# Performance work log

Hardware: AMD Instinct MI355X
Metric: run time of the kernel (lower is better)

Reference implementation:

```python
import jax, jax.numpy as jnp
import numpy as np

N_USER = 100000
N_ITEM = 100000
N_EDGE = 1600000
HID = 64
IN_U = 128
IN_I = 64
N_LAYERS = 2


def setup_inputs() -> dict:
    key = jax.random.key(0)
    ks = jax.random.split(key, 12)
    s = 0.05
    return {
        "x_user": jax.random.normal(ks[0], (N_USER, IN_U), jnp.float32),
        "x_item": jax.random.normal(ks[1], (N_ITEM, IN_I), jnp.float32),
        "edge_ui": jax.random.randint(ks[2], (2, N_EDGE), 0, N_USER),  # row0 src(user), row1 dst(item)
        "edge_iu": jax.random.randint(ks[3], (2, N_EDGE), 0, N_ITEM),  # row0 src(item), row1 dst(user)
        "Wu": jax.random.normal(ks[4], (IN_U, HID), jnp.float32) * s,
        "bu": jnp.zeros((HID,), jnp.float32),
        "Wi": jax.random.normal(ks[5], (IN_I, HID), jnp.float32) * s,
        "bi": jnp.zeros((HID,), jnp.float32),
        "Wl": jax.random.normal(ks[6], (N_LAYERS, 2, HID, HID), jnp.float32) * s,
        "bl": jnp.zeros((N_LAYERS, 2, HID), jnp.float32),
        "Wr": jax.random.normal(ks[7], (N_LAYERS, 2, HID, HID), jnp.float32) * s,
    }


def _sage(h_src, h_dst, edge, Wl, bl, Wr, n_dst):
    # SAGEConv: mean-aggregate gathered source features, then lin_l(agg)+bias + lin_r(dst)
    src, dst = edge[0], edge[1]
    msg = h_src[src]  # [E, HID] gather
    agg = jax.ops.segment_sum(msg, dst, num_segments=n_dst)
    cnt = jax.ops.segment_sum(jnp.ones((edge.shape[1], 1), h_src.dtype), dst, num_segments=n_dst)
    mean = agg / jnp.maximum(cnt, 1.0)
    return mean @ Wl + bl + h_dst @ Wr


def reference(x_user, x_item, edge_ui, edge_iu, Wu, bu, Wi, bi, Wl, bl, Wr):
    # per-node-type input linear + relu (dropout = identity at inference)
    hu = jax.nn.relu(x_user @ Wu + bu)
    hi = jax.nn.relu(x_item @ Wi + bi)
    for l in range(N_LAYERS):
        # edge type 0: user -> item ; edge type 1: item -> user ; HeteroConv aggr='sum'
        new_i = _sage(hu, hi, edge_ui, Wl[l, 0], bl[l, 0], Wr[l, 0], N_ITEM)
        new_u = _sage(hi, hu, edge_iu, Wl[l, 1], bl[l, 1], Wr[l, 1], N_USER)
        hu = jax.nn.relu(new_u)
        hi = jax.nn.relu(new_i)
    return hu, hi
```

## Files before the change

kernel.cpp:

```cpp
#include <hip/hip_runtime.h>

#define NUSER 100000
#define NITEM 100000
#define NEDGE 1600000
#define HID 64
#define NPB 256
#define NBKT 391
#define ACHUNK 8192
#define NCHUNK ((NEDGE + ACHUNK - 1) / ACHUNK)

__device__ __forceinline__ unsigned short f2bf(float x) {
  unsigned int u; __builtin_memcpy(&u, &x, 4);
  u += 0x7fffu + ((u >> 16) & 1u);
  return (unsigned short)(u >> 16);
}
__device__ __forceinline__ float bflo(unsigned int u) {
  unsigned int v = u << 16; float f; __builtin_memcpy(&f, &v, 4); return f;
}
__device__ __forceinline__ float bfhi(unsigned int u) {
  unsigned int v = u & 0xffff0000u; float f; __builtin_memcpy(&f, &v, 4); return f;
}

template<int K>
__global__ __launch_bounds__(256) void gemm64(
    const float* __restrict__ A, const float* __restrict__ W,
    const float* __restrict__ bias, float* __restrict__ C, int M)
{
  __shared__ float Ws[K * 64];
  __shared__ float As[64 * 68];
  const int tid = threadIdx.x;

  for (int i = tid; i < K * 16; i += 256)
    ((float4*)Ws)[i] = ((const float4*)W)[i];

  const int tx = tid & 15;
  const int ty = tid >> 4;
  float4 bv = ((const float4*)bias)[tx];

  const int ntiles = (M + 63) >> 6;
  for (int t = blockIdx.x; t < ntiles; t += gridDim.x) {
    const int row0 = t << 6;
    float acc[4][4] = {};
    for (int kb = 0; kb < K; kb += 64) {
      __syncthreads();
      for (int i = tid; i < 1024; i += 256) {
        int r = i >> 4;
        int kk = (i & 15) << 2;
        int gr = row0 + r; if (gr > M - 1) gr = M - 1;
        *(float4*)&As[r * 68 + kk] = *(const float4*)(A + (size_t)gr * K + kb + kk);
      }
      __syncthreads();
      #pragma unroll 8
      for (int k = 0; k < 64; ++k) {
        float4 w = *(const float4*)&Ws[(kb + k) * 64 + tx * 4];
        float a0 = As[(ty * 4 + 0) * 68 + k];
        float a1 = As[(ty * 4 + 1) * 68 + k];
        float a2 = As[(ty * 4 + 2) * 68 + k];
        float a3 = As[(ty * 4 + 3) * 68 + k];
        acc[0][0] += a0 * w.x; acc[0][1] += a0 * w.y; acc[0][2] += a0 * w.z; acc[0][3] += a0 * w.w;
        acc[1][0] += a1 * w.x; acc[1][1] += a1 * w.y; acc[1][2] += a1 * w.z; acc[1][3] += a1 * w.w;
        acc[2][0] += a2 * w.x; acc[2][1] += a2 * w.y; acc[2][2] += a2 * w.z; acc[2][3] += a2 * w.w;
        acc[3][0] += a3 * w.x; acc[3][1] += a3 * w.y; acc[3][2] += a3 * w.z; acc[3][3] += a3 * w.w;
      }
    }
    #pragma unroll
    for (int r = 0; r < 4; ++r) {
      int gr = row0 + ty * 4 + r;
      if (gr < M) {
        float4 o = make_float4(fmaxf(acc[r][0] + bv.x, 0.f), fmaxf(acc[r][1] + bv.y, 0.f),
                               fmaxf(acc[r][2] + bv.z, 0.f), fmaxf(acc[r][3] + bv.w, 0.f));
        *(float4*)(C + (size_t)gr * 64 + tx * 4) = o;
      }
    }
  }
}

__global__ __launch_bounds__(256) void gemm_dual2(
    const float* A0, const float* __restrict__ Wa0, const float* __restrict__ Wb0,
    const float* __restrict__ bias0, unsigned short* Ga0, float* Tb0,
    const float* A1, const float* __restrict__ Wa1, const float* __restrict__ Wb1,
    const float* __restrict__ bias1, unsigned short* Ga1, float* Tb1,
    int M, int half_blocks)
{
  __shared__ float Ws[64 * 128];
  __shared__ float As[64 * 68];
  const int tid = threadIdx.x;

  const float* A; const float* Wa; const float* Wb; const float* bias;
  unsigned short* Ga; float* Tb; int t;
  if ((int)blockIdx.x < half_blocks) {
    A = A0; Wa = Wa0; Wb = Wb0; bias = bias0; Ga = Ga0; Tb = Tb0; t = blockIdx.x;
  } else {
    A = A1; Wa = Wa1; Wb = Wb1; bias = bias1; Ga = Ga1; Tb = Tb1; t = blockIdx.x - half_blocks;
  }

  for (int i = tid; i < 2048; i += 256) {
    int k = i >> 5, cg = i & 31;
    float4 v = (cg < 16) ? ((const float4*)Wa)[k * 16 + cg]
                         : ((const float4*)Wb)[k * 16 + (cg - 16)];
    ((float4*)Ws)[k * 32 + cg] = v;
  }

  const int tx = tid & 15;
  const int ty = tid >> 4;
  float4 bvB = ((const float4*)bias)[tx];

  const int row0 = t << 6;
  float accA[4][4] = {};
  float accB[4][4] = {};
  __syncthreads();
  for (int i = tid; i < 1024; i += 256) {
    int r = i >> 4;
    int kk = (i & 15) << 2;
    int gr = row0 + r; if (gr > M - 1) gr = M - 1;
    *(float4*)&As[r * 68 + kk] = *(const float4*)(A + (size_t)gr * 64 + kk);
  }
  __syncthreads();
  #pragma unroll 8
  for (int k = 0; k < 64; ++k) {
    float4 wa = *(const float4*)&Ws[k * 128 + tx * 4];
    float4 wb = *(const float4*)&Ws[k * 128 + 64 + tx * 4];
    float a0 = As[(ty * 4 + 0) * 68 + k];
    float a1 = As[(ty * 4 + 1) * 68 + k];
    float a2 = As[(ty * 4 + 2) * 68 + k];
    float a3 = As[(ty * 4 + 3) * 68 + k];
    accA[0][0] += a0 * wa.x; accA[0][1] += a0 * wa.y; accA[0][2] += a0 * wa.z; accA[0][3] += a0 * wa.w;
    accA[1][0] += a1 * wa.x; accA[1][1] += a1 * wa.y; accA[1][2] += a1 * wa.z; accA[1][3] += a1 * wa.w;
    accA[2][0] += a2 * wa.x; accA[2][1] += a2 * wa.y; accA[2][2] += a2 * wa.z; accA[2][3] += a2 * wa.w;
    accA[3][0] += a3 * wa.x; accA[3][1] += a3 * wa.y; accA[3][2] += a3 * wa.z; accA[3][3] += a3 * wa.w;
    accB[0][0] += a0 * wb.x; accB[0][1] += a0 * wb.y; accB[0][2] += a0 * wb.z; accB[0][3] += a0 * wb.w;
    accB[1][0] += a1 * wb.x; accB[1][1] += a1 * wb.y; accB[1][2] += a1 * wb.z; accB[1][3] += a1 * wb.w;
    accB[2][0] += a2 * wb.x; accB[2][1] += a2 * wb.y; accB[2][2] += a2 * wb.z; accB[2][3] += a2 * wb.w;
    accB[3][0] += a3 * wb.x; accB[3][1] += a3 * wb.y; accB[3][2] += a3 * wb.z; accB[3][3] += a3 * wb.w;
  }
  #pragma unroll
  for (int r = 0; r < 4; ++r) {
    int gr = row0 + ty * 4 + r;
    if (gr < M) {
      ushort4 g;
      g.x = f2bf(accA[r][0]); g.y = f2bf(accA[r][1]);
      g.z = f2bf(accA[r][2]); g.w = f2bf(accA[r][3]);
      *(ushort4*)(Ga + (size_t)gr * 64 + tx * 4) = g;
      *(float4*)(Tb + (size_t)gr * 64 + tx * 4) =
          make_float4(accB[r][0] + bvB.x, accB[r][1] + bvB.y,
                      accB[r][2] + bvB.z, accB[r][3] + bvB.w);
    }
  }
}

__global__ __launch_bounds__(256) void agg2(
    const unsigned short* __restrict__ G0, const float* T0,
    const int* __restrict__ ptr0, const int* __restrict__ idx0, float* out0,
    const unsigned short* __restrict__ G1, const float* T1,
    const int* __restrict__ ptr1, const int* __restrict__ idx1, float* out1,
    int n_dst)
{
  const int lane = threadIdx.x & 63;
  const int sub = lane >> 5;
  const int ch = (lane & 31) << 1;
  int wave = blockIdx.x * 4 + (threadIdx.x >> 6);
  const int nwh = (gridDim.x * 4) >> 1;
  const unsigned short* G; const float* T; const int* ptr; const int* idx; float* out;
  if (wave < nwh) { G = G0; T = T0; ptr = ptr0; idx = idx0; out = out0; }
  else { G = G1; T = T1; ptr = ptr1; idx = idx1; out = out1; wave -= nwh; }

  for (int n0 = wave * 2; n0 < n_dst; n0 += nwh * 2) {
    const int n = n0 + sub;
    const bool valid = n < n_dst;
    const int s = valid ? ptr[n] : 0;
    const int e = valid ? ptr[n + 1] : 0;
    float2 t = make_float2(0.f, 0.f);
    if (valid) t = *(const float2*)(T + (size_t)n * 64 + ch);
    float l0 = 0.f, h0 = 0.f, l1 = 0.f, h1 = 0.f;
    float l2 = 0.f, h2 = 0.f, l3 = 0.f, h3 = 0.f;
    float l4 = 0.f, h4 = 0.f, l5 = 0.f, h5 = 0.f;
    float l6 = 0.f, h6 = 0.f, l7 = 0.f, h7 = 0.f;
    int i = s;
    for (; i + 8 <= e; i += 8) {
      int j0 = __builtin_nontemporal_load(idx + i + 0);
      int j1 = __builtin_nontemporal_load(idx + i + 1);
      int j2 = __builtin_nontemporal_load(idx + i + 2);
      int j3 = __builtin_nontemporal_load(idx + i + 3);
      int j4 = __builtin_nontemporal_load(idx + i + 4);
      int j5 = __builtin_nontemporal_load(idx + i + 5);
      int j6 = __builtin_nontemporal_load(idx + i + 6);
      int j7 = __builtin_nontemporal_load(idx + i + 7);
      unsigned int g0 = *(const unsigned int*)(G + (size_t)j0 * 64 + ch);
      unsigned int g1 = *(const unsigned int*)(G + (size_t)j1 * 64 + ch);
      unsigned int g2 = *(const unsigned int*)(G + (size_t)j2 * 64 + ch);
      unsigned int g3 = *(const unsigned int*)(G + (size_t)j3 * 64 + ch);
      unsigned int g4 = *(const unsigned int*)(G + (size_t)j4 * 64 + ch);
      unsigned int g5 = *(const unsigned int*)(G + (size_t)j5 * 64 + ch);
      unsigned int g6 = *(const unsigned int*)(G + (size_t)j6 * 64 + ch);
      unsigned int g7 = *(const unsigned int*)(G + (size_t)j7 * 64 + ch);
      l0 += bflo(g0); h0 += bfhi(g0); l1 += bflo(g1); h1 += bfhi(g1);
      l2 += bflo(g2); h2 += bfhi(g2); l3 += bflo(g3); h3 += bfhi(g3);
      l4 += bflo(g4); h4 += bfhi(g4); l5 += bflo(g5); h5 += bfhi(g5);
      l6 += bflo(g6); h6 += bfhi(g6); l7 += bflo(g7); h7 += bfhi(g7);
    }
    for (; i < e; ++i) {
      int j = __builtin_nontemporal_load(idx + i);
      unsigned int g = *(const unsigned int*)(G + (size_t)j * 64 + ch);
      l0 += bflo(g); h0 += bfhi(g);
    }
    float sl = ((l0 + l1) + (l2 + l3)) + ((l4 + l5) + (l6 + l7));
    float sh = ((h0 + h1) + (h2 + h3)) + ((h4 + h5) + (h6 + h7));
    int deg = e - s;
    float inv = 1.f / (float)(deg > 0 ? deg : 1);
    if (valid) {
      float2 o = make_float2(fmaxf(sl * inv + t.x, 0.f), fmaxf(sh * inv + t.y, 0.f));
      *(float2*)(out + (size_t)n * 64 + ch) = o;
    }
  }
}

__global__ __launch_bounds__(256) void bucket_hist(
    const int* __restrict__ dstA, const int* __restrict__ dstB,
    int* histA, int* histB, int E)
{
  __shared__ int h[NBKT];
  for (int i = threadIdx.x; i < NBKT; i += 256) h[i] = 0;
  __syncthreads();
  const int half = gridDim.x >> 1;
  const bool isB = (int)blockIdx.x >= half;
  const int* dst = isB ? dstB : dstA;
  int* hist = isB ? histB : histA;
  const int b0 = isB ? blockIdx.x - half : blockIdx.x;
  for (int e = b0 * 256 + (int)threadIdx.x; e < E; e += half * 256)
    atomicAdd(&h[__builtin_nontemporal_load(dst + e) >> 8], 1);
  __syncthreads();
  for (int i = threadIdx.x; i < NBKT; i += 256)
    if (h[i]) atomicAdd(&hist[i], h[i]);
}

__global__ __launch_bounds__(512) void bucket_scan(
    const int* __restrict__ histA, const int* __restrict__ histB,
    int* baseA, int* curA, int* baseB, int* curB,
    int* ptrA_end, int* ptrB_end, int E)
{
  __shared__ int sA[512], sB[512];
  const int t = threadIdx.x;
  int vA = (t < NBKT) ? histA[t] : 0;
  int vB = (t < NBKT) ? histB[t] : 0;
  sA[t] = vA; sB[t] = vB;
  __syncthreads();
  for (int off = 1; off < 512; off <<= 1) {
    int xA = 0, xB = 0;
    if (t >= off) { xA = sA[t - off]; xB = sB[t - off]; }
    __syncthreads();
    if (t >= off) { sA[t] += xA; sB[t] += xB; }
    __syncthreads();
  }
  if (t < NBKT) {
    int eA = sA[t] - vA, eB = sB[t] - vB;
    baseA[t] = eA; curA[t] = eA;
    baseB[t] = eB; curB[t] = eB;
  }
  if (t == 0) {
    baseA[NBKT] = E; baseB[NBKT] = E;
    *ptrA_end = E; *ptrB_end = E;
  }
}

__global__ __launch_bounds__(256) void partition2(
    const int* __restrict__ srcA, const int* __restrict__ dstA, int* curA, unsigned int* pairsA,
    const int* __restrict__ srcB, const int* __restrict__ dstB, int* curB, unsigned int* pairsB,
    int E)
{
  __shared__ int h[NBKT];
  __shared__ int c[NBKT];
  const int half = gridDim.x >> 1;
  const bool isB = (int)blockIdx.x >= half;
  const int chunk = isB ? blockIdx.x - half : blockIdx.x;
  const int* src = isB ? srcB : srcA;
  const int* dst = isB ? dstB : dstA;
  int* cur = isB ? curB : curA;
  unsigned int* pairs = isB ? pairsB : pairsA;
  const int e0 = chunk * ACHUNK;
  const int e1 = min(e0 + ACHUNK, E);
  for (int i = threadIdx.x; i < NBKT; i += 256) h[i] = 0;
  __syncthreads();
  for (int e = e0 + (int)threadIdx.x; e < e1; e += 256)
    atomicAdd(&h[__builtin_nontemporal_load(dst + e) >> 8], 1);
  __syncthreads();
  for (int i = threadIdx.x; i < NBKT; i += 256) {
    int v = h[i];
    if (v) c[i] = atomicAdd(&cur[i], v);
  }
  __syncthreads();
  for (int e = e0 + (int)threadIdx.x; e < e1; e += 256) {
    int d = __builtin_nontemporal_load(dst + e);
    int s = __builtin_nontemporal_load(src + e);
    int b = d >> 8;
    int p = atomicAdd(&c[b], 1);
    pairs[p] = ((unsigned int)(d & 255) << 24) | (unsigned int)s;
  }
}

__global__ __launch_bounds__(256) void bucket_fill(
    const unsigned int* __restrict__ pairsA, const int* __restrict__ baseA,
    int* __restrict__ ptrA, int* __restrict__ idxA,
    const unsigned int* __restrict__ pairsB, const int* __restrict__ baseB,
    int* __restrict__ ptrB, int* __restrict__ idxB, int n)
{
  __shared__ int h[NPB];
  __shared__ int cur[NPB];
  const bool isB = (int)blockIdx.x >= NBKT;
  const int b = isB ? blockIdx.x - NBKT : blockIdx.x;
  const unsigned int* pairs = isB ? pairsB : pairsA;
  const int* base = isB ? baseB : baseA;
  int* ptr = isB ? ptrB : ptrA;
  int* idx = isB ? idxB : idxA;
  const int ebase = base[b];
  const int eend = base[b + 1];
  const int t = threadIdx.x;
  h[t] = 0;
  __syncthreads();
  for (int e = ebase + t; e < eend; e += 256)
    atomicAdd(&h[pairs[e] >> 24], 1);
  __syncthreads();
  const int v = h[t];
  __syncthreads();
  for (int off = 1; off < 256; off <<= 1) {
    int x = 0;
    if (t >= off) x = h[t - off];
    __syncthreads();
    if (t >= off) h[t] += x;
    __syncthreads();
  }
  const int excl = h[t] - v;
  const int gnode = b * NPB + t;
  if (gnode < n) ptr[gnode] = ebase + excl;
  cur[t] = excl;
  __syncthreads();
  for (int e = ebase + t; e < eend; e += 256) {
    unsigned int pk = pairs[e];
    int p = atomicAdd(&cur[pk >> 24], 1);
    idx[ebase + p] = (int)(pk & 0xFFFFFFu);
  }
}

extern "C" void kernel_launch(void* const* d_in, const int* in_sizes, int n_in,
                              void* d_out, int out_size, void* d_ws, size_t ws_size,
                              hipStream_t stream) {
  const float* x_user = (const float*)d_in[0];
  const float* x_item = (const float*)d_in[1];
  const int*   edge_ui = (const int*)d_in[2];
  const int*   edge_iu = (const int*)d_in[3];
  const float* Wu = (const float*)d_in[4];
  const float* bu = (const float*)d_in[5];
  const float* Wi = (const float*)d_in[6];
  const float* bi = (const float*)d_in[7];
  const float* Wl = (const float*)d_in[8];
  const float* bl = (const float*)d_in[9];
  const float* Wr = (const float*)d_in[10];

  float* outU = (float*)d_out;
  float* outI = outU + (size_t)NUSER * HID;

  char* p = (char*)d_ws;
  auto alloc = [&](size_t bytes) -> void* {
    void* r = (void*)p; p += (bytes + 255) & ~(size_t)255; return r;
  };
  float* U = (float*)alloc((size_t)NUSER * HID * 4);
  float* I = (float*)alloc((size_t)NITEM * HID * 4);
  unsigned short* GA = (unsigned short*)alloc((size_t)NUSER * HID * 2);
  unsigned short* GB = (unsigned short*)alloc((size_t)NITEM * HID * 2);
  unsigned int* pairsA = (unsigned int*)GA;
  unsigned int* pairsB = pairsA + NEDGE;
  int* histA = (int*)alloc((size_t)(2 * NBKT + 2 * (NBKT + 1) + 2 * NBKT) * 4);
  int* histB = histA + NBKT;
  int* baseA = histB + NBKT;
  int* baseB = baseA + NBKT + 1;
  int* curA  = baseB + NBKT + 1;
  int* curB  = curA + NBKT;
  int* ptr_ui = (int*)alloc(((size_t)NITEM + 1) * 4);
  int* ptr_iu = (int*)alloc(((size_t)NUSER + 1) * 4);
  int* idx_ui = (int*)alloc((size_t)NEDGE * 4);
  int* idx_iu = (int*)alloc((size_t)NEDGE * 4);

  hipMemsetAsync(histA, 0, (size_t)(2 * NBKT) * 4, stream);
  bucket_hist<<<784, 256, 0, stream>>>(edge_ui + NEDGE, edge_iu + NEDGE,
                                       histA, histB, NEDGE);
  bucket_scan<<<1, 512, 0, stream>>>(histA, histB, baseA, curA, baseB, curB,
                                     ptr_ui + NITEM, ptr_iu + NUSER, NEDGE);
  partition2<<<2 * NCHUNK, 256, 0, stream>>>(
      edge_ui, edge_ui + NEDGE, curA, pairsA,
      edge_iu, edge_iu + NEDGE, curB, pairsB, NEDGE);
  bucket_fill<<<2 * NBKT, 256, 0, stream>>>(pairsA, baseA, ptr_ui, idx_ui,
                                            pairsB, baseB, ptr_iu, idx_iu, NITEM);

  const int GT = (NUSER + 63) / 64;
  const int AGG_B = 2 * ((NUSER / 2 + 3) / 4);

  const float* Wl00 = Wl;             const float* Wl01 = Wl + 4096;
  const float* Wl10 = Wl + 2 * 4096;  const float* Wl11 = Wl + 3 * 4096;
  const float* Wr00 = Wr;             const float* Wr01 = Wr + 4096;
  const float* Wr10 = Wr + 2 * 4096;  const float* Wr11 = Wr + 3 * 4096;
  const float* bl00 = bl;             const float* bl01 = bl + 64;
  const float* bl10 = bl + 128;       const float* bl11 = bl + 192;

  gemm64<128><<<GT, 256, 0, stream>>>(x_user, Wu, bu, U, NUSER);
  gemm64<64 ><<<GT, 256, 0, stream>>>(x_item, Wi, bi, I, NITEM);

  gemm_dual2<<<2 * GT, 256, 0, stream>>>(U, Wl00, Wr01, bl01, GA, outU,
                                         I, Wl01, Wr00, bl00, GB, outI,
                                         NUSER, GT);
  agg2<<<AGG_B, 256, 0, stream>>>(GA, outI, ptr_ui, idx_ui, outI,
                                  GB, outU, ptr_iu, idx_iu, outU, NITEM);

  gemm_dual2<<<2 * GT, 256, 0, stream>>>(outI, Wl11, Wr10, bl10, GA, outI,
                                         outU, Wl10, Wr11, bl11, GB, outU,
                                         NITEM, GT);
  agg2<<<AGG_B, 256, 0, stream>>>(GA, outU, ptr_iu, idx_iu, outU,
                                  GB, outI, ptr_ui, idx_ui, outI, NUSER);
}
```

Baseline: 609.2 us.

## Schedule aggregation by XCD affinity with atomic work-stealing chunks

Replaces the static split of waves between the two edge directions with dynamic chunk claiming through per-side global atomic counters. Each block reads its XCD id and processes the side assigned to its XCD half first, so each half of the chip keeps one gathered feature table hot in its L2 before switching to the other side. This adds an atomic plus two block barriers per 64-node chunk and relies on the hardware XCC_ID register.

```diff
diff --git a/kernel.cpp b/kernel.cpp
--- a/kernel.cpp
+++ b/kernel.cpp
@@ -8,6 +8,7 @@
 #define NBKT 391
 #define ACHUNK 8192
 #define NCHUNK ((NEDGE + ACHUNK - 1) / ACHUNK)
+#define AGGCH 64
 
 __device__ __forceinline__ unsigned short f2bf(float x) {
   unsigned int u; __builtin_memcpy(&u, &x, 4);
@@ -19,6 +20,11 @@
 }
 __device__ __forceinline__ float bfhi(unsigned int u) {
   unsigned int v = u & 0xffff0000u; float f; __builtin_memcpy(&f, &v, 4); return f;
+}
+__device__ __forceinline__ int xcd_id() {
+  int x;
+  asm volatile("s_getreg_b32 %0, hwreg(HW_REG_XCC_ID)" : "=s"(x));
+  return x & 7;
 }
 
 template<int K>
@@ -153,63 +159,80 @@
     const int* __restrict__ ptr0, const int* __restrict__ idx0, float* out0,
     const unsigned short* __restrict__ G1, const float* T1,
     const int* __restrict__ ptr1, const int* __restrict__ idx1, float* out1,
-    int n_dst)
+    int* wc, int n_dst)
 {
   const int lane = threadIdx.x & 63;
   const int sub = lane >> 5;
   const int ch = (lane & 31) << 1;
-  int wave = blockIdx.x * 4 + (threadIdx.x >> 6);
-  const int nwh = (gridDim.x * 4) >> 1;
-  const unsigned short* G; const float* T; const int* ptr; const int* idx; float* out;
-  if (wave < nwh) { G = G0; T = T0; ptr = ptr0; idx = idx0; out = out0; }
-  else { G = G1; T = T1; ptr = ptr1; idx = idx1; out = out1; wave -= nwh; }
-
-  for (int n0 = wave * 2; n0 < n_dst; n0 += nwh * 2) {
-    const int n = n0 + sub;
-    const bool valid = n < n_dst;
-    const int s = valid ? ptr[n] : 0;
-    const int e = valid ? ptr[n + 1] : 0;
-    float2 t = make_float2(0.f, 0.f);
-    if (valid) t = *(const float2*)(T + (size_t)n * 64 + ch);
-    float l0 = 0.f, h0 = 0.f, l1 = 0.f, h1 = 0.f;
-    float l2 = 0.f, h2 = 0.f, l3 = 0.f, h3 = 0.f;
-    float l4 = 0.f, h4 = 0.f, l5 = 0.f, h5 = 0.f;
-    float l6 = 0.f, h6 = 0.f, l7 = 0.f, h7 = 0.f;
-    int i = s;
-    for (; i + 8 <= e; i += 8) {
-      int j0 = __builtin_nontemporal_load(idx + i + 0);
-      int j1 = __builtin_nontemporal_load(idx + i + 1);
-      int j2 = __builtin_nontemporal_load(idx + i + 2);
-      int j3 = __builtin_nontemporal_load(idx + i + 3);
-      int j4 = __builtin_nontemporal_load(idx + i + 4);
-      int j5 = __builtin_nontemporal_load(idx + i + 5);
-      int j6 = __builtin_nontemporal_load(idx + i + 6);
-      int j7 = __builtin_nontemporal_load(idx + i + 7);
-      unsigned int g0 = *(const unsigned int*)(G + (size_t)j0 * 64 + ch);
-      unsigned int g1 = *(const unsigned int*)(G + (size_t)j1 * 64 + ch);
-      unsigned int g2 = *(const unsigned int*)(G + (size_t)j2 * 64 + ch);
-      unsigned int g3 = *(const unsigned int*)(G + (size_t)j3 * 64 + ch);
-      unsigned int g4 = *(const unsigned int*)(G + (size_t)j4 * 64 + ch);
-      unsigned int g5 = *(const unsigned int*)(G + (size_t)j5 * 64 + ch);
-      unsigned int g6 = *(const unsigned int*)(G + (size_t)j6 * 64 + ch);
-      unsigned int g7 = *(const unsigned int*)(G + (size_t)j7 * 64 + ch);
-      l0 += bflo(g0); h0 += bfhi(g0); l1 += bflo(g1); h1 += bfhi(g1);
-      l2 += bflo(g2); h2 += bfhi(g2); l3 += bflo(g3); h3 += bfhi(g3);
-      l4 += bflo(g4); h4 += bfhi(g4); l5 += bflo(g5); h5 += bfhi(g5);
-      l6 += bflo(g6); h6 += bfhi(g6); l7 += bflo(g7); h7 += bfhi(g7);
-    }
-    for (; i < e; ++i) {
-      int j = __builtin_nontemporal_load(idx + i);
-      unsigned int g = *(const unsigned int*)(G + (size_t)j * 64 + ch);
-      l0 += bflo(g); h0 += bfhi(g);
-    }
-    float sl = ((l0 + l1) + (l2 + l3)) + ((l4 + l5) + (l6 + l7));
-    float sh = ((h0 + h1) + (h2 + h3)) + ((h4 + h5) + (h6 + h7));
-    int deg = e - s;
-    float inv = 1.f / (float)(deg > 0 ? deg : 1);
-    if (valid) {
-      float2 o = make_float2(fmaxf(sl * inv + t.x, 0.f), fmaxf(sh * inv + t.y, 0.f));
-      *(float2*)(out + (size_t)n * 64 + ch) = o;
+  const int slot = ((threadIdx.x >> 6) << 1) | sub;
+  const int nchk = (n_dst + AGGCH - 1) / AGGCH;
+  const int g = xcd_id();
+  __shared__ int s_c;
+
+  for (int pass = 0; pass < 2; ++pass) {
+    const int side = ((g >> 2) ^ pass) & 1;
+    const unsigned short* G = side ? G1 : G0;
+    const float* T = side ? T1 : T0;
+    const int* ptr = side ? ptr1 : ptr0;
+    const int* idx = side ? idx1 : idx0;
+    float* out = side ? out1 : out0;
+    int* cnt = wc + side;
+    for (;;) {
+      if (threadIdx.x == 0) s_c = atomicAdd(cnt, 1);
+      __syncthreads();
+      const int c = s_c;
+      __syncthreads();
+      if (c >= nchk) break;
+      const int base = c * AGGCH;
+      #pragma unroll 1
+      for (int it = 0; it < AGGCH / 8; ++it) {
+        const int n = base + it * 8 + slot;
+        const bool valid = n < n_dst;
+        const int s = valid ? ptr[n] : 0;
+        const int e = valid ? ptr[n + 1] : 0;
+        float2 t = make_float2(0.f, 0.f);
+        if (valid) t = *(const float2*)(T + (size_t)n * 64 + ch);
+        float l0 = 0.f, h0 = 0.f, l1 = 0.f, h1 = 0.f;
+        float l2 = 0.f, h2 = 0.f, l3 = 0.f, h3 = 0.f;
+        float l4 = 0.f, h4 = 0.f, l5 = 0.f, h5 = 0.f;
+        float l6 = 0.f, h6 = 0.f, l7 = 0.f, h7 = 0.f;
+        int i = s;
+        for (; i + 8 <= e; i += 8) {
+          int j0 = __builtin_nontemporal_load(idx + i + 0);
+          int j1 = __builtin_nontemporal_load(idx + i + 1);
+          int j2 = __builtin_nontemporal_load(idx + i + 2);
+          int j3 = __builtin_nontemporal_load(idx + i + 3);
+          int j4 = __builtin_nontemporal_load(idx + i + 4);
+          int j5 = __builtin_nontemporal_load(idx + i + 5);
+          int j6 = __builtin_nontemporal_load(idx + i + 6);
+          int j7 = __builtin_nontemporal_load(idx + i + 7);
+          unsigned int g0 = *(const unsigned int*)(G + (size_t)j0 * 64 + ch);
+          unsigned int g1 = *(const unsigned int*)(G + (size_t)j1 * 64 + ch);
+          unsigned int g2 = *(const unsigned int*)(G + (size_t)j2 * 64 + ch);
+          unsigned int g3 = *(const unsigned int*)(G + (size_t)j3 * 64 + ch);
+          unsigned int g4 = *(const unsigned int*)(G + (size_t)j4 * 64 + ch);
+          unsigned int g5 = *(const unsigned int*)(G + (size_t)j5 * 64 + ch);
+          unsigned int g6 = *(const unsigned int*)(G + (size_t)j6 * 64 + ch);
+          unsigned int g7 = *(const unsigned int*)(G + (size_t)j7 * 64 + ch);
+          l0 += bflo(g0); h0 += bfhi(g0); l1 += bflo(g1); h1 += bfhi(g1);
+          l2 += bflo(g2); h2 += bfhi(g2); l3 += bflo(g3); h3 += bfhi(g3);
+          l4 += bflo(g4); h4 += bfhi(g4); l5 += bflo(g5); h5 += bfhi(g5);
+          l6 += bflo(g6); h6 += bfhi(g6); l7 += bflo(g7); h7 += bfhi(g7);
+        }
+        for (; i < e; ++i) {
+          int j = __builtin_nontemporal_load(idx + i);
+          unsigned int gv = *(const unsigned int*)(G + (size_t)j * 64 + ch);
+          l0 += bflo(gv); h0 += bfhi(gv);
+        }
+        float sl = ((l0 + l1) + (l2 + l3)) + ((l4 + l5) + (l6 + l7));
+        float sh = ((h0 + h1) + (h2 + h3)) + ((h4 + h5) + (h6 + h7));
+        int deg = e - s;
+        float inv = 1.f / (float)(deg > 0 ? deg : 1);
+        if (valid) {
+          float2 o = make_float2(fmaxf(sl * inv + t.x, 0.f), fmaxf(sh * inv + t.y, 0.f));
+          *(float2*)(out + (size_t)n * 64 + ch) = o;
+        }
+      }
     }
   }
 }
@@ -368,9 +391,10 @@
   unsigned short* GB = (unsigned short*)alloc((size_t)NITEM * HID * 2);
   unsigned int* pairsA = (unsigned int*)GA;
   unsigned int* pairsB = pairsA + NEDGE;
-  int* histA = (int*)alloc((size_t)(2 * NBKT + 2 * (NBKT + 1) + 2 * NBKT) * 4);
+  int* histA = (int*)alloc((size_t)(2 * NBKT + 8 + 2 * (NBKT + 1) + 2 * NBKT) * 4);
   int* histB = histA + NBKT;
-  int* baseA = histB + NBKT;
+  int* wc    = histA + 2 * NBKT;
+  int* baseA = wc + 8;
   int* baseB = baseA + NBKT + 1;
   int* curA  = baseB + NBKT + 1;
   int* curB  = curA + NBKT;
@@ -379,7 +403,7 @@
   int* idx_ui = (int*)alloc((size_t)NEDGE * 4);
   int* idx_iu = (int*)alloc((size_t)NEDGE * 4);
 
-  hipMemsetAsync(histA, 0, (size_t)(2 * NBKT) * 4, stream);
+  hipMemsetAsync(histA, 0, (size_t)(2 * NBKT + 8) * 4, stream);
   bucket_hist<<<784, 256, 0, stream>>>(edge_ui + NEDGE, edge_iu + NEDGE,
                                        histA, histB, NEDGE);
   bucket_scan<<<1, 512, 0, stream>>>(histA, histB, baseA, curA, baseB, curB,
@@ -391,7 +415,6 @@
                                             pairsB, baseB, ptr_iu, idx_iu, NITEM);
 
   const int GT = (NUSER + 63) / 64;
-  const int AGG_B = 2 * ((NUSER / 2 + 3) / 4);
 
   const float* Wl00 = Wl;             const float* Wl01 = Wl + 4096;
   const float* Wl10 = Wl + 2 * 4096;  const float* Wl11 = Wl + 3 * 4096;
@@ -406,12 +429,12 @@
   gemm_dual2<<<2 * GT, 256, 0, stream>>>(U, Wl00, Wr01, bl01, GA, outU,
                                          I, Wl01, Wr00, bl00, GB, outI,
                                          NUSER, GT);
-  agg2<<<AGG_B, 256, 0, stream>>>(GA, outI, ptr_ui, idx_ui, outI,
-                                  GB, outU, ptr_iu, idx_iu, outU, NITEM);
+  agg2<<<2048, 256, 0, stream>>>(GA, outI, ptr_ui, idx_ui, outI,
+                                 GB, outU, ptr_iu, idx_iu, outU, wc + 0, NITEM);
 
   gemm_dual2<<<2 * GT, 256, 0, stream>>>(outI, Wl11, Wr10, bl10, GA, outI,
                                          outU, Wl10, Wr11, bl11, GB, outU,
                                          NITEM, GT);
-  agg2<<<AGG_B, 256, 0, stream>>>(GA, outU, ptr_iu, idx_iu, outU,
-                                  GB, outI, ptr_ui, idx_ui, outI, NUSER);
-}
+  agg2<<<2048, 256, 0, stream>>>(GA, outU, ptr_iu, idx_iu, outU,
+                                 GB, outI, ptr_ui, idx_ui, outI, wc + 4, NUSER);
+}
```

Measured after the change: 728.0 us. +19.5%, slower.
